# Optimization experiments

Measured on AMD Instinct MI355X. Metric: run time of the kernel, lower is better.

## Reference

```python
import jax, jax.numpy as jnp
import numpy as np

B, C, D_IN, D_H, D_OUT = 131072, 16, 256, 1024, 256


def setup_inputs() -> dict:
    key = jax.random.key(0)
    k = jax.random.split(key, 6)
    return {
        "x": jax.random.normal(k[0], (B, D_IN), dtype=jnp.float32),
        "cat_ids": jax.random.randint(k[1], (B,), 0, C, dtype=jnp.int32),
        "W1": jax.random.normal(k[2], (C, D_IN, D_H), dtype=jnp.float32) * (1.0 / np.sqrt(D_IN)),
        "b1": jax.random.normal(k[3], (C, D_H), dtype=jnp.float32) * 0.02,
        "W2": jax.random.normal(k[4], (C, D_H, D_OUT), dtype=jnp.float32) * (1.0 / np.sqrt(D_H)),
        "b2": jax.random.normal(k[5], (C, D_OUT), dtype=jnp.float32) * 0.02,
    }


def _routed_linear(x, cat_ids, W, b):
    # Category-routed linear: out[i] = x[i] @ W[cat_ids[i]] + b[cat_ids[i]].
    # Loop over the small fixed category count (not over tokens); each branch
    # is a dense GEMM masked by the routing assignment. This is equivalent to
    # the original gather -> per-category Linear -> scatter/argsort pattern
    # without materializing per-token weight gathers.
    num_categories = W.shape[0]
    out = jnp.zeros((x.shape[0], W.shape[2]), dtype=x.dtype)
    for c in range(num_categories):
        mask = (cat_ids == c)[:, None]
        out = out + jnp.where(mask, x @ W[c] + b[c], jnp.zeros((), x.dtype))
    return out


def reference(x, cat_ids, W1, b1, W2, b2):
    hidden = jax.nn.relu(_routed_linear(x, cat_ids, W1, b1))
    return _routed_linear(hidden, cat_ids, W2, b2)
```

## Files before the change

### kernel.cpp

```cpp
#include <hip/hip_runtime.h>
#include <hip/hip_bf16.h>

#define BB   131072
#define CC   16
#define DIN  256
#define DH   1024
#define DOUT 256
#define TM   64
#define NHB  32
#define NB   512

typedef __attribute__((ext_vector_type(8))) short bf16x8;
typedef __attribute__((ext_vector_type(4))) short short4v;
typedef __attribute__((ext_vector_type(4))) float f32x4;

__device__ inline unsigned short f2b(float f) {
  union { float f; unsigned u; } v; v.f = f;
  unsigned u = v.u;
  return (unsigned short)((u + 0x7fffu + ((u >> 16) & 1u)) >> 16);
}

__device__ inline void gload_lds16(const void* g, void* l) {
  __builtin_amdgcn_global_load_lds(
      (const __attribute__((address_space(1))) void*)g,
      (__attribute__((address_space(3))) void*)l, 16, 0, 0);
}

#define MFMA16(a, b, c) __builtin_amdgcn_mfma_f32_16x16x32_bf16((a), (b), (c), 0, 0, 0)

__global__ void hist_k(const int* __restrict__ cat, int* __restrict__ blockhist) {
  __shared__ int h[CC];
  const int tid = threadIdx.x;
  if (tid < CC) h[tid] = 0;
  __syncthreads();
  const int i = blockIdx.x * 256 + tid;
  atomicAdd(&h[cat[i]], 1);
  __syncthreads();
  if (tid < CC) blockhist[blockIdx.x * CC + tid] = h[tid];
}

__global__ void offsets2_k(const int* __restrict__ blockhist,
                           int* __restrict__ counts, int* __restrict__ padoff,
                           int* __restrict__ base) {
  __shared__ int part[CC][64];
  __shared__ int pref[CC][64];
  __shared__ int scnt[CC];
  __shared__ int spad[CC + 1];
  const int tid = threadIdx.x;
  const int c = tid >> 6;
  const int g = tid & 63;
  int h[8];
  int s = 0;
#pragma unroll
  for (int i = 0; i < 8; i++) {
    h[i] = blockhist[(g * 8 + i) * CC + c];
    s += h[i];
  }
  part[c][g] = s;
  __syncthreads();
  if (g == 0) {
    int r = 0;
    for (int j = 0; j < 64; j++) { pref[c][j] = r; r += part[c][j]; }
    scnt[c] = r;
  }
  __syncthreads();
  if (tid == 0) {
    int acc = 0;
    for (int c2 = 0; c2 < CC; c2++) {
      spad[c2] = acc;
      padoff[c2] = acc;
      counts[c2] = scnt[c2];
      acc += ((scnt[c2] + TM - 1) / TM) * TM;
    }
    spad[CC] = acc;
    padoff[CC] = acc;
  }
  __syncthreads();
  int run = spad[c] + pref[c][g];
#pragma unroll
  for (int i = 0; i < 8; i++) {
    base[(g * 8 + i) * CC + c] = run;
    run += h[i];
  }
}

__global__ void scatter2_k(const int* __restrict__ cat, const int* __restrict__ base,
                           int* __restrict__ idx) {
  __shared__ int cur[CC];
  const int tid = threadIdx.x;
  if (tid < CC) cur[tid] = base[blockIdx.x * CC + tid];
  __syncthreads();
  const int i = blockIdx.x * 256 + tid;
  const int c = cat[i];
  const int pos = atomicAdd(&cur[c], 1);
  idx[pos] = i;
}

__global__ void conv_w1_k(const float* __restrict__ W1, short* __restrict__ w1b) {
  int t = blockIdx.x * blockDim.x + threadIdx.x;
  int n  = t & 1023;
  int j8 = (t >> 10) & 31;
  int c  = t >> 15;
  const float* src = W1 + (size_t)c * DIN * DH;
  bf16x8 o;
#pragma unroll
  for (int i = 0; i < 8; i++)
    o[i] = (short)f2b(src[(size_t)(j8 * 8 + i) * DH + n]);
  char* dst = (char*)w1b + (size_t)c * 524288
            + (n >> 5) * 16384 + ((n >> 4) & 1) * 8192 + (j8 >> 2) * 1024
            + ((n & 15) + 16 * (j8 & 3)) * 16;
  *(bf16x8*)dst = o;
}

__global__ void conv_w2_k(const float* __restrict__ W2, short* __restrict__ w2b) {
  int t = blockIdx.x * blockDim.x + threadIdx.x;
  int n  = t & 255;
  int j8 = (t >> 8) & 127;
  int c  = t >> 15;
  const float* src = W2 + (size_t)c * DH * DOUT;
  bf16x8 o;
#pragma unroll
  for (int i = 0; i < 8; i++)
    o[i] = (short)f2b(src[(size_t)(j8 * 8 + i) * DOUT + n]);
  char* dst = (char*)w2b + (size_t)c * 524288
            + (j8 >> 2) * 16384 + (n >> 4) * 1024
            + ((n & 15) + 16 * (j8 & 3)) * 16;
  *(bf16x8*)dst = o;
}

#define W2OFF  16384
#define HSOFF  32768
#define TKOFF  36864
#define B1OFF  37120
#define B2OFF  41216
#define SMSZ   42240

__launch_bounds__(256, 3)
__global__ void mlp_k(const float* __restrict__ x,
                      const float* __restrict__ b1,
                      const float* __restrict__ b2,
                      const short* __restrict__ w1b,
                      const short* __restrict__ w2b,
                      const int* __restrict__ idx,
                      const int* __restrict__ padoff,
                      const int* __restrict__ counts,
                      float* __restrict__ out) {
  __shared__ __align__(16) char sm[SMSZ];

  const int bhw = blockIdx.x;
  const int wg = (bhw & 7) * 258 + (bhw >> 3);
  const int p = wg * TM;
  const int total = padoff[CC];
  if (p >= total) return;
  int c = 0;
  while (padoff[c + 1] <= p) c++;
  const int cnt = counts[c];
  const int start = p - padoff[c];

  const int tid  = threadIdx.x;
  const int lane = tid & 63;
  const int w    = tid >> 6;
  const int wt   = w >> 1;
  const int wh   = w & 1;
  const int lrow = lane & 15;
  const int lgrp = lane >> 4;

  char*  hsb   = sm + HSOFF;
  int*   toksp = (int*)(sm + TKOFF);
  float* b1s   = (float*)(sm + B1OFF);
  float* b2s   = (float*)(sm + B2OFF);

  {
    const int r = tid >> 2;
    const int q = tid & 3;
    const int pos = start + r;
    int tok = (pos < cnt) ? idx[p + r] : -1;
    if (q == 0) toksp[r] = tok;
    char* tb = sm + (r >> 4) * 8192 + (r & 15) * 16;
    if (tok >= 0) {
      const f32x4* src = (const f32x4*)(x + (size_t)tok * DIN) + q * 16;
#pragma unroll
      for (int t = 0; t < 8; t++) {
        f32x4 v0 = src[2 * t];
        f32x4 v1 = src[2 * t + 1];
        bf16x8 o;
        o[0] = (short)f2b(v0[0]); o[1] = (short)f2b(v0[1]);
        o[2] = (short)f2b(v0[2]); o[3] = (short)f2b(v0[3]);
        o[4] = (short)f2b(v1[0]); o[5] = (short)f2b(v1[1]);
        o[6] = (short)f2b(v1[2]); o[7] = (short)f2b(v1[3]);
        *(bf16x8*)(tb + (2 * q + (t >> 2)) * 1024 + (t & 3) * 256) = o;
      }
    } else {
      bf16x8 z = {0, 0, 0, 0, 0, 0, 0, 0};
#pragma unroll
      for (int t = 0; t < 8; t++)
        *(bf16x8*)(tb + (2 * q + (t >> 2)) * 1024 + (t & 3) * 256) = z;
    }
    ((f32x4*)b1s)[tid] = ((const f32x4*)(b1 + (size_t)c * DH))[tid];
    if (tid < 64) ((f32x4*)b2s)[tid] = ((const f32x4*)(b2 + (size_t)c * DOUT))[tid];
  }
  __syncthreads();

  bf16x8 xf[2][8];
#pragma unroll
  for (int ti = 0; ti < 2; ti++)
#pragma unroll
    for (int ks = 0; ks < 8; ks++)
      xf[ti][ks] = *(const bf16x8*)(sm + (2 * wt + ti) * 8192 + ks * 1024 + lane * 16);
  __syncthreads();

  const char* w1g = (const char*)w1b + (size_t)c * 524288;
  const char* w2g = (const char*)w2b + (size_t)c * 524288;

  auto stage1 = [&](int i) {
    const char* src = w1g + (size_t)i * 16384;
#pragma unroll
    for (int j = 0; j < 4; j++) {
      int chunk = (w * 4 + j) * 1024;
      gload_lds16(src + chunk + lane * 16, sm + chunk);
    }
  };
  auto stage2 = [&](int i) {
    const char* src = w2g + (size_t)i * 16384;
#pragma unroll
    for (int j = 0; j < 4; j++) {
      int chunk = (w * 4 + j) * 1024;
      gload_lds16(src + chunk + lane * 16, sm + W2OFF + chunk);
    }
  };

  stage1(0);
  asm volatile("s_waitcnt vmcnt(0)" ::: "memory");
  __syncthreads();

  f32x4 acc2[2][8];
#pragma unroll
  for (int ti = 0; ti < 2; ti++)
#pragma unroll
    for (int ni = 0; ni < 8; ni++)
      acc2[ti][ni] = (f32x4){0.f, 0.f, 0.f, 0.f};

  const int hswr = (lrow + 16 * (wh * 2 + (lgrp >> 1))) * 16 + (lgrp & 1) * 8;
  const char* w1c = sm + wh * 8192;
  const char* w2c = sm + W2OFF;

  for (int hb = 0; hb < NHB; hb++) {
    const bool notlast = (hb < NHB - 1);

    stage2(hb);

    f32x4 p0 = (f32x4){0.f, 0.f, 0.f, 0.f};
    f32x4 p1 = (f32x4){0.f, 0.f, 0.f, 0.f};
    __builtin_amdgcn_s_setprio(1);
#pragma unroll
    for (int ks = 0; ks < 8; ks++) {
      bf16x8 a = *(const bf16x8*)(w1c + ks * 1024 + lane * 16);
      p0 = MFMA16(a, xf[0][ks], p0);
      p1 = MFMA16(a, xf[1][ks], p1);
    }
    __builtin_amdgcn_s_setprio(0);

    {
      f32x4 bv = *(const f32x4*)(b1s + hb * 32 + wh * 16 + lgrp * 4);
      short4v h0, h1;
#pragma unroll
      for (int jj = 0; jj < 4; jj++) {
        h0[jj] = (short)f2b(fmaxf(p0[jj] + bv[jj], 0.0f));
        h1[jj] = (short)f2b(fmaxf(p1[jj] + bv[jj], 0.0f));
      }
      *(short4v*)(hsb + (2 * wt) * 1024 + hswr)     = h0;
      *(short4v*)(hsb + (2 * wt + 1) * 1024 + hswr) = h1;
    }
    asm volatile("s_waitcnt vmcnt(0) lgkmcnt(0)" ::: "memory");
    __builtin_amdgcn_s_barrier();

    if (notlast) stage1(hb + 1);

    {
      bf16x8 hf0 = *(const bf16x8*)(hsb + (2 * wt) * 1024 + lane * 16);
      bf16x8 hf1 = *(const bf16x8*)(hsb + (2 * wt + 1) * 1024 + lane * 16);
      __builtin_amdgcn_s_setprio(1);
#pragma unroll
      for (int ni = 0; ni < 8; ni++) {
        bf16x8 a2 = *(const bf16x8*)(w2c + (wh * 8 + ni) * 1024 + lane * 16);
        acc2[0][ni] = MFMA16(a2, hf0, acc2[0][ni]);
        acc2[1][ni] = MFMA16(a2, hf1, acc2[1][ni]);
      }
      __builtin_amdgcn_s_setprio(0);
    }
    if (notlast) {
      asm volatile("s_waitcnt vmcnt(0) lgkmcnt(0)" ::: "memory");
      __builtin_amdgcn_s_barrier();
    }
  }

#pragma unroll
  for (int ti = 0; ti < 2; ti++) {
    const int tok = toksp[(2 * wt + ti) * 16 + lrow];
    if (tok >= 0) {
#pragma unroll
      for (int ni = 0; ni < 8; ni++) {
        const int n0 = wh * 128 + ni * 16 + lgrp * 4;
        f32x4 bv = *(const f32x4*)(b2s + n0);
        f32x4 v = acc2[ti][ni] + bv;
        *(f32x4*)(out + (size_t)tok * DOUT + n0) = v;
      }
    }
  }
}

extern "C" void kernel_launch(void* const* d_in, const int* in_sizes, int n_in,
                              void* d_out, int out_size, void* d_ws, size_t ws_size,
                              hipStream_t stream) {
  (void)in_sizes; (void)n_in; (void)out_size; (void)ws_size;
  const float* x   = (const float*)d_in[0];
  const int*   cat = (const int*)d_in[1];
  const float* W1  = (const float*)d_in[2];
  const float* b1  = (const float*)d_in[3];
  const float* W2  = (const float*)d_in[4];
  const float* b2  = (const float*)d_in[5];
  float* out = (float*)d_out;

  char* ws = (char*)d_ws;
  int* counts    = (int*)(ws);
  int* padoff    = (int*)(ws + 128);
  int* blockhist = (int*)(ws + 4096);
  int* base      = (int*)(ws + 65536);
  int* idx       = (int*)(ws + 131072);
  short* w1b     = (short*)(ws + (1 << 20));
  short* w2b     = (short*)(ws + (1 << 20) + 8388608);

  hist_k<<<NB, 256, 0, stream>>>(cat, blockhist);
  offsets2_k<<<1, 1024, 0, stream>>>(blockhist, counts, padoff, base);
  scatter2_k<<<NB, 256, 0, stream>>>(cat, base, idx);
  conv_w1_k<<<2048, 256, 0, stream>>>(W1, w1b);
  conv_w2_k<<<2048, 256, 0, stream>>>(W2, w2b);

  const int ntiles = BB / TM + CC;
  mlp_k<<<ntiles, 256, 0, stream>>>(x, b1, b2, w1b, w2b, idx, padoff, counts, out);
}
```

Measured before the change: 218.3 us.

## Split fused routed MLP into two passes with bf16 hidden in workspace

Replaces the single fused MLP kernel with two kernels when the workspace is large enough. The first pass computes ReLU(x@W1+b1) for 128-token tiles and writes the hidden activations as bf16 to global memory in an MFMA-friendly layout. The second pass streams them back with double-buffered W2 tiles to produce the output. Both use 512-thread blocks and larger tiles, trading the fused kernel's on-chip hidden reuse for simpler per-kernel pipelines. The cost is a large extra global write and read of the hidden tensor, plus a dependence on workspace size. The original fused path remains as a fallback.

```diff
diff --git a/kernel.cpp b/kernel.cpp
--- a/kernel.cpp
+++ b/kernel.cpp
@@ -6,8 +6,6 @@
 #define DIN  256
 #define DH   1024
 #define DOUT 256
-#define TM   64
-#define NHB  32
 #define NB   512
 
 typedef __attribute__((ext_vector_type(8))) short bf16x8;
@@ -41,7 +39,7 @@
 
 __global__ void offsets2_k(const int* __restrict__ blockhist,
                            int* __restrict__ counts, int* __restrict__ padoff,
-                           int* __restrict__ base) {
+                           int* __restrict__ base, int tm) {
   __shared__ int part[CC][64];
   __shared__ int pref[CC][64];
   __shared__ int scnt[CC];
@@ -70,7 +68,7 @@
       spad[c2] = acc;
       padoff[c2] = acc;
       counts[c2] = scnt[c2];
-      acc += ((scnt[c2] + TM - 1) / TM) * TM;
+      acc += ((scnt[c2] + tm - 1) / tm) * tm;
     }
     spad[CC] = acc;
     padoff[CC] = acc;
@@ -107,7 +105,7 @@
   for (int i = 0; i < 8; i++)
     o[i] = (short)f2b(src[(size_t)(j8 * 8 + i) * DH + n]);
   char* dst = (char*)w1b + (size_t)c * 524288
-            + (n >> 5) * 16384 + ((n >> 4) & 1) * 8192 + (j8 >> 2) * 1024
+            + (n >> 4) * 8192 + (j8 >> 2) * 1024
             + ((n & 15) + 16 * (j8 & 3)) * 16;
   *(bf16x8*)dst = o;
 }
@@ -128,12 +126,276 @@
   *(bf16x8*)dst = o;
 }
 
-#define W2OFF  16384
-#define HSOFF  32768
-#define TKOFF  36864
-#define B1OFF  37120
-#define B2OFF  41216
-#define SMSZ   42240
+#define P1TK   65536
+#define P1B1   66048
+#define P1SM   70144
+
+__launch_bounds__(512, 4)
+__global__ void p1_k(const float* __restrict__ x,
+                     const float* __restrict__ b1,
+                     const short* __restrict__ w1b,
+                     const int* __restrict__ idx,
+                     const int* __restrict__ padoff,
+                     const int* __restrict__ counts,
+                     char* __restrict__ hid) {
+  __shared__ __align__(16) char sm[P1SM];
+
+  const int bhw = blockIdx.x;
+  const int wg = (bhw & 7) * 130 + (bhw >> 3);
+  const int p = wg * 128;
+  const int total = padoff[CC];
+  if (p >= total) return;
+  int c = 0;
+  while (padoff[c + 1] <= p) c++;
+  const int cnt = counts[c];
+  const int start = p - padoff[c];
+
+  const int tid  = threadIdx.x;
+  const int lane = tid & 63;
+  const int w    = tid >> 6;
+  const int wt   = w >> 1;
+  const int wh   = w & 1;
+  const int lrow = lane & 15;
+  const int lgrp = lane >> 4;
+
+  int*   toksp = (int*)(sm + P1TK);
+  float* b1s   = (float*)(sm + P1B1);
+
+  {
+    const int r = tid >> 2;
+    const int q = tid & 3;
+    const int pos = start + r;
+    int tok = (pos < cnt) ? idx[p + r] : -1;
+    if (q == 0) toksp[r] = tok;
+    char* tb = sm + (r >> 4) * 8192 + (r & 15) * 16;
+    if (tok >= 0) {
+      const f32x4* src = (const f32x4*)(x + (size_t)tok * DIN) + q * 16;
+#pragma unroll
+      for (int t = 0; t < 8; t++) {
+        f32x4 v0 = src[2 * t];
+        f32x4 v1 = src[2 * t + 1];
+        bf16x8 o;
+        o[0] = (short)f2b(v0[0]); o[1] = (short)f2b(v0[1]);
+        o[2] = (short)f2b(v0[2]); o[3] = (short)f2b(v0[3]);
+        o[4] = (short)f2b(v1[0]); o[5] = (short)f2b(v1[1]);
+        o[6] = (short)f2b(v1[2]); o[7] = (short)f2b(v1[3]);
+        *(bf16x8*)(tb + (2 * q + (t >> 2)) * 1024 + (t & 3) * 256) = o;
+      }
+    } else {
+      bf16x8 z = {0, 0, 0, 0, 0, 0, 0, 0};
+#pragma unroll
+      for (int t = 0; t < 8; t++)
+        *(bf16x8*)(tb + (2 * q + (t >> 2)) * 1024 + (t & 3) * 256) = z;
+    }
+    if (tid < 256) ((f32x4*)b1s)[tid] = ((const f32x4*)(b1 + (size_t)c * DH))[tid];
+  }
+  __syncthreads();
+
+  bf16x8 xf[2][8];
+#pragma unroll
+  for (int ti = 0; ti < 2; ti++)
+#pragma unroll
+    for (int ks = 0; ks < 8; ks++)
+      xf[ti][ks] = *(const bf16x8*)(sm + (2 * wt + ti) * 8192 + ks * 1024 + lane * 16);
+  __syncthreads();
+
+  const char* w1g = (const char*)w1b + (size_t)c * 524288;
+  auto stage1 = [&](int i) {
+    const char* src = w1g + (size_t)i * 32768;
+    char* dst = sm + (i & 1) * 32768;
+#pragma unroll
+    for (int j = 0; j < 4; j++) {
+      int chunk = (w * 4 + j) * 1024;
+      gload_lds16(src + chunk + lane * 16, dst + chunk);
+    }
+  };
+
+  stage1(0);
+  asm volatile("s_waitcnt vmcnt(0)" ::: "memory");
+  __syncthreads();
+
+  const int hp = (lrow + 16 * (lgrp >> 1)) * 16 + (lgrp & 1) * 8;
+  char* hb0 = hid + ((size_t)(wg * 8 + 2 * wt)) * 32768;
+  char* hb1 = hid + ((size_t)(wg * 8 + 2 * wt + 1)) * 32768;
+
+  for (int hb = 0; hb < 16; hb++) {
+    const bool notlast = (hb < 15);
+    const char* w1c = sm + (hb & 1) * 32768;
+    if (notlast) stage1(hb + 1);
+
+    f32x4 acc1[2][2];
+#pragma unroll
+    for (int ti = 0; ti < 2; ti++)
+#pragma unroll
+      for (int nj = 0; nj < 2; nj++)
+        acc1[ti][nj] = (f32x4){0.f, 0.f, 0.f, 0.f};
+
+    __builtin_amdgcn_s_setprio(1);
+#pragma unroll
+    for (int ks = 0; ks < 8; ks++) {
+      bf16x8 a0 = *(const bf16x8*)(w1c + (2 * wh + 0) * 8192 + ks * 1024 + lane * 16);
+      bf16x8 a1 = *(const bf16x8*)(w1c + (2 * wh + 1) * 8192 + ks * 1024 + lane * 16);
+      acc1[0][0] = MFMA16(a0, xf[0][ks], acc1[0][0]);
+      acc1[1][0] = MFMA16(a0, xf[1][ks], acc1[1][0]);
+      acc1[0][1] = MFMA16(a1, xf[0][ks], acc1[0][1]);
+      acc1[1][1] = MFMA16(a1, xf[1][ks], acc1[1][1]);
+    }
+    __builtin_amdgcn_s_setprio(0);
+
+    const int kboff = (hb * 2 + wh) * 1024;
+#pragma unroll
+    for (int nj = 0; nj < 2; nj++) {
+      f32x4 bv = *(const f32x4*)(b1s + hb * 64 + (2 * wh + nj) * 16 + lgrp * 4);
+      short4v h0, h1;
+#pragma unroll
+      for (int jj = 0; jj < 4; jj++) {
+        h0[jj] = (short)f2b(fmaxf(acc1[0][nj][jj] + bv[jj], 0.0f));
+        h1[jj] = (short)f2b(fmaxf(acc1[1][nj][jj] + bv[jj], 0.0f));
+      }
+      *(short4v*)(hb0 + kboff + hp + nj * 512) = h0;
+      *(short4v*)(hb1 + kboff + hp + nj * 512) = h1;
+    }
+
+    if (notlast) {
+      asm volatile("s_waitcnt vmcnt(4)" ::: "memory");
+      __builtin_amdgcn_s_barrier();
+    }
+  }
+}
+
+#define P2TK   32768
+#define P2B2   33280
+#define P2SM   34304
+
+__launch_bounds__(512, 4)
+__global__ void p2_k(const float* __restrict__ b2,
+                     const short* __restrict__ w2b,
+                     const int* __restrict__ idx,
+                     const int* __restrict__ padoff,
+                     const int* __restrict__ counts,
+                     const char* __restrict__ hid,
+                     float* __restrict__ out) {
+  __shared__ __align__(16) char sm[P2SM];
+
+  const int bhw = blockIdx.x;
+  const int wg = (bhw & 7) * 130 + (bhw >> 3);
+  const int p = wg * 128;
+  const int total = padoff[CC];
+  if (p >= total) return;
+  int c = 0;
+  while (padoff[c + 1] <= p) c++;
+  const int cnt = counts[c];
+  const int start = p - padoff[c];
+
+  const int tid  = threadIdx.x;
+  const int lane = tid & 63;
+  const int w    = tid >> 6;
+  const int wt   = w >> 1;
+  const int wh   = w & 1;
+  const int lrow = lane & 15;
+  const int lgrp = lane >> 4;
+
+  int*   toksp = (int*)(sm + P2TK);
+  float* b2s   = (float*)(sm + P2B2);
+
+  if (tid < 128) {
+    const int pos = start + tid;
+    toksp[tid] = (pos < cnt) ? idx[p + tid] : -1;
+  }
+  if (tid < 64) ((f32x4*)b2s)[tid] = ((const f32x4*)(b2 + (size_t)c * DOUT))[tid];
+
+  const char* w2g = (const char*)w2b + (size_t)c * 524288;
+  auto stage2 = [&](int i) {
+    const char* src = w2g + (size_t)i * 16384;
+    char* dst = sm + (i & 1) * 16384;
+#pragma unroll
+    for (int j = 0; j < 2; j++) {
+      int chunk = (w * 2 + j) * 1024;
+      gload_lds16(src + chunk + lane * 16, dst + chunk);
+    }
+  };
+
+  const char* h0 = hid + ((size_t)(wg * 8 + 2 * wt)) * 32768 + lane * 16;
+  const char* h1 = hid + ((size_t)(wg * 8 + 2 * wt + 1)) * 32768 + lane * 16;
+
+  f32x4 acc2[2][8];
+#pragma unroll
+  for (int ti = 0; ti < 2; ti++)
+#pragma unroll
+    for (int ni = 0; ni < 8; ni++)
+      acc2[ti][ni] = (f32x4){0.f, 0.f, 0.f, 0.f};
+
+  __syncthreads();
+  stage2(0);
+  bf16x8 hfA0 = *(const bf16x8*)(h0);
+  bf16x8 hfA1 = *(const bf16x8*)(h1);
+  asm volatile("s_waitcnt vmcnt(0)" ::: "memory");
+  __builtin_amdgcn_s_barrier();
+
+  bf16x8 hfB0, hfB1;
+#pragma unroll
+  for (int kb = 0; kb < 32; kb += 2) {
+    {
+      stage2(kb + 1);
+      hfB0 = *(const bf16x8*)(h0 + (kb + 1) * 1024);
+      hfB1 = *(const bf16x8*)(h1 + (kb + 1) * 1024);
+      const char* w2c = sm;
+      __builtin_amdgcn_s_setprio(1);
+#pragma unroll
+      for (int ni = 0; ni < 8; ni++) {
+        bf16x8 a2 = *(const bf16x8*)(w2c + (wh * 8 + ni) * 1024 + lane * 16);
+        acc2[0][ni] = MFMA16(a2, hfA0, acc2[0][ni]);
+        acc2[1][ni] = MFMA16(a2, hfA1, acc2[1][ni]);
+      }
+      __builtin_amdgcn_s_setprio(0);
+      asm volatile("s_waitcnt vmcnt(0) lgkmcnt(0)" ::: "memory");
+      __builtin_amdgcn_s_barrier();
+    }
+    {
+      const bool more = (kb + 2 < 32);
+      if (more) {
+        stage2(kb + 2);
+        hfA0 = *(const bf16x8*)(h0 + (kb + 2) * 1024);
+        hfA1 = *(const bf16x8*)(h1 + (kb + 2) * 1024);
+      }
+      const char* w2c = sm + 16384;
+      __builtin_amdgcn_s_setprio(1);
+#pragma unroll
+      for (int ni = 0; ni < 8; ni++) {
+        bf16x8 a2 = *(const bf16x8*)(w2c + (wh * 8 + ni) * 1024 + lane * 16);
+        acc2[0][ni] = MFMA16(a2, hfB0, acc2[0][ni]);
+        acc2[1][ni] = MFMA16(a2, hfB1, acc2[1][ni]);
+      }
+      __builtin_amdgcn_s_setprio(0);
+      if (more) {
+        asm volatile("s_waitcnt vmcnt(0) lgkmcnt(0)" ::: "memory");
+        __builtin_amdgcn_s_barrier();
+      }
+    }
+  }
+
+#pragma unroll
+  for (int ti = 0; ti < 2; ti++) {
+    const int tok = toksp[(2 * wt + ti) * 16 + lrow];
+    if (tok >= 0) {
+#pragma unroll
+      for (int ni = 0; ni < 8; ni++) {
+        const int n0 = wh * 128 + ni * 16 + lgrp * 4;
+        f32x4 bv = *(const f32x4*)(b2s + n0);
+        f32x4 v = acc2[ti][ni] + bv;
+        *(f32x4*)(out + (size_t)tok * DOUT + n0) = v;
+      }
+    }
+  }
+}
+
+#define FTM   64
+#define FW2   16384
+#define FHS   32768
+#define FTK   36864
+#define FB1   37120
+#define FB2   41216
+#define FSM   42240
 
 __launch_bounds__(256, 3)
 __global__ void mlp_k(const float* __restrict__ x,
@@ -145,11 +407,11 @@
                       const int* __restrict__ padoff,
                       const int* __restrict__ counts,
                       float* __restrict__ out) {
-  __shared__ __align__(16) char sm[SMSZ];
+  __shared__ __align__(16) char sm[FSM];
 
   const int bhw = blockIdx.x;
   const int wg = (bhw & 7) * 258 + (bhw >> 3);
-  const int p = wg * TM;
+  const int p = wg * FTM;
   const int total = padoff[CC];
   if (p >= total) return;
   int c = 0;
@@ -165,10 +427,10 @@
   const int lrow = lane & 15;
   const int lgrp = lane >> 4;
 
-  char*  hsb   = sm + HSOFF;
-  int*   toksp = (int*)(sm + TKOFF);
-  float* b1s   = (float*)(sm + B1OFF);
-  float* b2s   = (float*)(sm + B2OFF);
+  char*  hsb   = sm + FHS;
+  int*   toksp = (int*)(sm + FTK);
+  float* b1s   = (float*)(sm + FB1);
+  float* b2s   = (float*)(sm + FB2);
 
   {
     const int r = tid >> 2;
@@ -225,7 +487,7 @@
 #pragma unroll
     for (int j = 0; j < 4; j++) {
       int chunk = (w * 4 + j) * 1024;
-      gload_lds16(src + chunk + lane * 16, sm + W2OFF + chunk);
+      gload_lds16(src + chunk + lane * 16, sm + FW2 + chunk);
     }
   };
 
@@ -242,11 +504,10 @@
 
   const int hswr = (lrow + 16 * (wh * 2 + (lgrp >> 1))) * 16 + (lgrp & 1) * 8;
   const char* w1c = sm + wh * 8192;
-  const char* w2c = sm + W2OFF;
-
-  for (int hb = 0; hb < NHB; hb++) {
-    const bool notlast = (hb < NHB - 1);
-
+  const char* w2c = sm + FW2;
+
+  for (int hb = 0; hb < 32; hb++) {
+    const bool notlast = (hb < 31);
     stage2(hb);
 
     f32x4 p0 = (f32x4){0.f, 0.f, 0.f, 0.f};
@@ -275,7 +536,6 @@
     __builtin_amdgcn_s_barrier();
 
     if (notlast) stage1(hb + 1);
-
     {
       bf16x8 hf0 = *(const bf16x8*)(hsb + (2 * wt) * 1024 + lane * 16);
       bf16x8 hf1 = *(const bf16x8*)(hsb + (2 * wt + 1) * 1024 + lane * 16);
@@ -312,7 +572,7 @@
 extern "C" void kernel_launch(void* const* d_in, const int* in_sizes, int n_in,
                               void* d_out, int out_size, void* d_ws, size_t ws_size,
                               hipStream_t stream) {
-  (void)in_sizes; (void)n_in; (void)out_size; (void)ws_size;
+  (void)in_sizes; (void)n_in; (void)out_size;
   const float* x   = (const float*)d_in[0];
   const int*   cat = (const int*)d_in[1];
   const float* W1  = (const float*)d_in[2];
@@ -329,13 +589,23 @@
   int* idx       = (int*)(ws + 131072);
   short* w1b     = (short*)(ws + (1 << 20));
   short* w2b     = (short*)(ws + (1 << 20) + 8388608);
+  char* hid      = ws + 18874368;
+
+  const int nt1 = BB / 128 + CC;
+  const size_t need = 18874368ull + (size_t)nt1 * 8 * 32768ull;
+  const bool twopass = (ws_size >= need);
 
   hist_k<<<NB, 256, 0, stream>>>(cat, blockhist);
-  offsets2_k<<<1, 1024, 0, stream>>>(blockhist, counts, padoff, base);
+  offsets2_k<<<1, 1024, 0, stream>>>(blockhist, counts, padoff, base, twopass ? 128 : FTM);
   scatter2_k<<<NB, 256, 0, stream>>>(cat, base, idx);
   conv_w1_k<<<2048, 256, 0, stream>>>(W1, w1b);
   conv_w2_k<<<2048, 256, 0, stream>>>(W2, w2b);
 
-  const int ntiles = BB / TM + CC;
-  mlp_k<<<ntiles, 256, 0, stream>>>(x, b1, b2, w1b, w2b, idx, padoff, counts, out);
-}
+  if (twopass) {
+    p1_k<<<nt1, 512, 0, stream>>>(x, b1, w1b, idx, padoff, counts, hid);
+    p2_k<<<nt1, 512, 0, stream>>>(b2, w2b, idx, padoff, counts, hid, out);
+  } else {
+    const int ntf = BB / FTM + CC;
+    mlp_k<<<ntf, 256, 0, stream>>>(x, b1, b2, w1b, w2b, idx, padoff, counts, out);
+  }
+}
```

Result: slower. 299.1 us (+37.1%).
